# Optimization experiments

Measured on AMD Instinct MI355X. Metric: run time of the kernel, lower is better.

## Reference

```python
import jax, jax.numpy as jnp
import numpy as np

EPS = 1e-16


def setup_inputs() -> dict:
    key = jax.random.key(0)
    k1, k2 = jax.random.split(key)
    p = jax.random.normal(k1, (2, 32, 2048, 4), dtype=jnp.float32)
    q = jax.random.normal(k2, (32, 2048, 4), dtype=jnp.float32)
    return {"p": p, "q": q}


def reference(p, q):
    # im=False path: take the real part of the complex generated momenta
    p_real = p[0]                      # (B, N, 4)
    # loss_norm_choice='p3', take_sqrt=True: use 3-momenta (drop energy)
    p3 = p_real[..., 1:]               # (B, N, 3)
    q3 = q[..., 1:]                    # (B, M, 3)
    # Pairwise Euclidean distance (cdist) via the expanded quadratic form to
    # avoid materializing the (B, N, M, 3) difference tensor.
    x2 = jnp.sum(p3 * p3, axis=-1)     # (B, N)
    y2 = jnp.sum(q3 * q3, axis=-1)     # (B, M)
    xy = jnp.einsum('bnd,bmd->bnm', p3, q3)  # (B, N, M)
    dist_sq = x2[..., :, None] + y2[..., None, :] - 2.0 * xy
    dist = jnp.sqrt(jnp.maximum(dist_sq, 0.0) + EPS)  # (B, N, M)
    # Bidirectional nearest-neighbor min-reduction
    min_pq = jnp.min(dist, axis=-1)    # (B, N)
    min_qp = jnp.min(dist, axis=-2)    # (B, M)
    chamfer_loss = jnp.sum((min_pq + min_qp) * 0.5)
    return chamfer_loss
```

## Files before the change

kernel.cpp:

```cpp
#include <hip/hip_runtime.h>
#include <math.h>


#define NPTS   2048
#define NBATCH 32
#define NBI    16
#define NBJ    16
#define WS_ROW_FLOATS ((size_t)NBATCH * NBI * NBJ * 128)
#define EPSF   1e-16f
#define BIGF   3.4e38f

__device__ __forceinline__ float min3f(float a, float b, float c) {
    return fminf(fminf(a, b), c);
}

__global__ __launch_bounds__(256) void chamfer_tile_kernel(
    const float* __restrict__ P, const float* __restrict__ Q,
    float* __restrict__ ws)
{
    __shared__ float4 sq[128];
    __shared__ float  scol[4][128];
    __shared__ float  rrow[128];

    const int tid  = threadIdx.x;
    const int tx   = tid & 15;
    const int ty   = tid >> 4;
    const int lane = tid & 63;
    const int wv   = tid >> 6;
    const int bi   = blockIdx.x;
    const int bj   = blockIdx.y;
    const int b    = blockIdx.z;

    if (tid < 128) {
        float4 qv = ((const float4*)Q)[(size_t)b * NPTS + bj * 128 + tid];
        sq[tid] = make_float4(-2.f * qv.y, -2.f * qv.z, -2.f * qv.w,
                              qv.y * qv.y + qv.z * qv.z + qv.w * qv.w);
    }

    const float4* Pb = (const float4*)P + (size_t)b * NPTS + (size_t)bi * 128;
    float px[8], py[8], pz[8], x2[8], rowacc[8];
    #pragma unroll
    for (int k = 0; k < 8; ++k) {
        float4 v = Pb[ty + 16 * k];
        px[k] = v.y; py[k] = v.z; pz[k] = v.w;
        x2[k] = v.y * v.y + v.z * v.z + v.w * v.w;
        rowacc[k] = BIGF;
    }
    __syncthreads();

    float4 qr[8];
    #pragma unroll
    for (int j = 0; j < 8; ++j) qr[j] = sq[tx + 16 * j];

    float colacc[8];
    #pragma unroll
    for (int jp = 0; jp < 4; ++jp) {
        float4 q0 = qr[2 * jp];
        float4 q1 = qr[2 * jp + 1];
        float c0 = BIGF, c1 = BIGF;
        #pragma unroll
        for (int k = 0; k < 8; k += 2) {
            float t00 = fmaf(px[k],   q0.x, fmaf(py[k],   q0.y, pz[k]   * q0.z));
            float t01 = fmaf(px[k],   q1.x, fmaf(py[k],   q1.y, pz[k]   * q1.z));
            float t10 = fmaf(px[k+1], q0.x, fmaf(py[k+1], q0.y, pz[k+1] * q0.z));
            float t11 = fmaf(px[k+1], q1.x, fmaf(py[k+1], q1.y, pz[k+1] * q1.z));
            rowacc[k]   = min3f(rowacc[k],   t00 + q0.w, t01 + q1.w);
            rowacc[k+1] = min3f(rowacc[k+1], t10 + q0.w, t11 + q1.w);
            c0 = min3f(c0, t00 + x2[k], t10 + x2[k+1]);
            c1 = min3f(c1, t01 + x2[k], t11 + x2[k+1]);
        }
        colacc[2*jp]     = c0;
        colacc[2*jp + 1] = c1;
    }

    #pragma unroll
    for (int k = 0; k < 8; ++k) {
        float v = rowacc[k];
        v = fminf(v, __shfl_xor(v, 1));
        v = fminf(v, __shfl_xor(v, 2));
        v = fminf(v, __shfl_xor(v, 4));
        v = fminf(v, __shfl_xor(v, 8));
        if (tx == 0) rrow[ty + 16 * k] = x2[k] + v;
    }

    #pragma unroll
    for (int j = 0; j < 8; ++j) {
        float v = colacc[j];
        v = fminf(v, __shfl_xor(v, 16));
        v = fminf(v, __shfl_xor(v, 32));
        colacc[j] = v;
    }
    if (lane < 16) {
        #pragma unroll
        for (int j = 0; j < 8; ++j) scol[wv][j * 16 + lane] = colacc[j];
    }
    __syncthreads();

    if (tid < 128) {
        float v = fminf(fminf(scol[0][tid], scol[1][tid]),
                        fminf(scol[2][tid], scol[3][tid]));
        float* wsC = ws + WS_ROW_FLOATS;
        wsC[(((size_t)b * NBJ + bj) * NBI + bi) * 128 + tid] = v + sq[tid].w;
        ws[(((size_t)b * NBI + bi) * NBJ + bj) * 128 + tid] = rrow[tid];
    }
}

__global__ __launch_bounds__(256) void chamfer_finish_kernel(
    const float* __restrict__ ws, float* __restrict__ out)
{
    __shared__ float rbuf[4];
    const int tid = threadIdx.x;
    const int i   = blockIdx.x * 256 + tid;
    const int b   = i >> 11;
    const int e   = i & 2047;
    const int ch  = e >> 7;
    const int el  = e & 127;

    float s;
    {
        const float* rb = ws + ((size_t)(b * NBI + ch) * NBJ) * 128 + el;
        float v = BIGF;
        #pragma unroll
        for (int j = 0; j < NBJ; ++j) v = fminf(v, rb[j * 128]);
        s = sqrtf(fmaxf(v, 0.f) + EPSF);
    }
    {
        const float* cb = ws + WS_ROW_FLOATS
                        + ((size_t)(b * NBJ + ch) * NBI) * 128 + el;
        float v = BIGF;
        #pragma unroll
        for (int j = 0; j < NBI; ++j) v = fminf(v, cb[j * 128]);
        s += sqrtf(fmaxf(v, 0.f) + EPSF);
    }

    #pragma unroll
    for (int off = 32; off > 0; off >>= 1) s += __shfl_down(s, off);
    if ((tid & 63) == 0) rbuf[tid >> 6] = s;
    __syncthreads();
    if (tid == 0)
        atomicAdd(out, 0.5f * ((rbuf[0] + rbuf[1]) + (rbuf[2] + rbuf[3])));
}

extern "C" void kernel_launch(void* const* d_in, const int* in_sizes, int n_in,
                              void* d_out, int out_size, void* d_ws, size_t ws_size,
                              hipStream_t stream) {
    const float* P = (const float*)d_in[0];
    const float* Q = (const float*)d_in[1];
    float* out = (float*)d_out;
    float* ws  = (float*)d_ws;

    hipMemsetAsync(out, 0, sizeof(float), stream);
    dim3 grid(NBI, NBJ, NBATCH);
    chamfer_tile_kernel<<<grid, 256, 0, stream>>>(P, Q, ws);
    chamfer_finish_kernel<<<256, 256, 0, stream>>>(ws, out);
}
```

Measured before the change: 95.54 us.

## Loop each block over eight P tiles, keeping Q tile and column minima in registers

Each block now keeps one 128-point Q tile in registers and loops over eight P tiles (half of the points), instead of handling a single 128x128 tile. Column minima build up across the loop, so only two column partials per Q tile go to the workspace, and the finish kernel reduces two values instead of sixteen. The grid shrinks from 8192 blocks to 1024, which cuts block launch and Q reload overhead and folds x2 into the FMA chain, but lowers parallelism and serializes the P loads within each block.

```diff
diff --git a/kernel.cpp b/kernel.cpp
--- a/kernel.cpp
+++ b/kernel.cpp
@@ -6,6 +6,7 @@
 #define NBATCH 32
 #define NBI    16
 #define NBJ    16
+#define NHALF  2
 #define WS_ROW_FLOATS ((size_t)NBATCH * NBI * NBJ * 128)
 #define EPSF   1e-16f
 #define BIGF   3.4e38f
@@ -14,21 +15,20 @@
     return fminf(fminf(a, b), c);
 }
 
-__global__ __launch_bounds__(256) void chamfer_tile_kernel(
+__global__ __launch_bounds__(256, 4) void chamfer_tile_kernel(
     const float* __restrict__ P, const float* __restrict__ Q,
     float* __restrict__ ws)
 {
     __shared__ float4 sq[128];
     __shared__ float  scol[4][128];
-    __shared__ float  rrow[128];
 
     const int tid  = threadIdx.x;
     const int tx   = tid & 15;
     const int ty   = tid >> 4;
     const int lane = tid & 63;
     const int wv   = tid >> 6;
-    const int bi   = blockIdx.x;
-    const int bj   = blockIdx.y;
+    const int bj   = blockIdx.x;
+    const int half = blockIdx.y;
     const int b    = blockIdx.z;
 
     if (tid < 128) {
@@ -36,51 +36,61 @@
         sq[tid] = make_float4(-2.f * qv.y, -2.f * qv.z, -2.f * qv.w,
                               qv.y * qv.y + qv.z * qv.z + qv.w * qv.w);
     }
-
-    const float4* Pb = (const float4*)P + (size_t)b * NPTS + (size_t)bi * 128;
-    float px[8], py[8], pz[8], x2[8], rowacc[8];
-    #pragma unroll
-    for (int k = 0; k < 8; ++k) {
-        float4 v = Pb[ty + 16 * k];
-        px[k] = v.y; py[k] = v.z; pz[k] = v.w;
-        x2[k] = v.y * v.y + v.z * v.z + v.w * v.w;
-        rowacc[k] = BIGF;
-    }
     __syncthreads();
 
-    float4 qr[8];
+    float qx[8], qy[8], qz[8], qw[8], colacc[8];
     #pragma unroll
-    for (int j = 0; j < 8; ++j) qr[j] = sq[tx + 16 * j];
-
-    float colacc[8];
-    #pragma unroll
-    for (int jp = 0; jp < 4; ++jp) {
-        float4 q0 = qr[2 * jp];
-        float4 q1 = qr[2 * jp + 1];
-        float c0 = BIGF, c1 = BIGF;
-        #pragma unroll
-        for (int k = 0; k < 8; k += 2) {
-            float t00 = fmaf(px[k],   q0.x, fmaf(py[k],   q0.y, pz[k]   * q0.z));
-            float t01 = fmaf(px[k],   q1.x, fmaf(py[k],   q1.y, pz[k]   * q1.z));
-            float t10 = fmaf(px[k+1], q0.x, fmaf(py[k+1], q0.y, pz[k+1] * q0.z));
-            float t11 = fmaf(px[k+1], q1.x, fmaf(py[k+1], q1.y, pz[k+1] * q1.z));
-            rowacc[k]   = min3f(rowacc[k],   t00 + q0.w, t01 + q1.w);
-            rowacc[k+1] = min3f(rowacc[k+1], t10 + q0.w, t11 + q1.w);
-            c0 = min3f(c0, t00 + x2[k], t10 + x2[k+1]);
-            c1 = min3f(c1, t01 + x2[k], t11 + x2[k+1]);
-        }
-        colacc[2*jp]     = c0;
-        colacc[2*jp + 1] = c1;
+    for (int j = 0; j < 8; ++j) {
+        float4 t = sq[tx + 16 * j];
+        qx[j] = t.x; qy[j] = t.y; qz[j] = t.z; qw[j] = t.w;
+        colacc[j] = BIGF;
     }
 
-    #pragma unroll
-    for (int k = 0; k < 8; ++k) {
-        float v = rowacc[k];
-        v = fminf(v, __shfl_xor(v, 1));
-        v = fminf(v, __shfl_xor(v, 2));
-        v = fminf(v, __shfl_xor(v, 4));
-        v = fminf(v, __shfl_xor(v, 8));
-        if (tx == 0) rrow[ty + 16 * k] = x2[k] + v;
+    const float4* Pb = (const float4*)P + (size_t)b * NPTS
+                     + (size_t)half * (NPTS / 2);
+
+    for (int it = 0; it < 8; ++it) {
+        const int bi = half * 8 + it;
+
+        float px[8], py[8], pz[8], x2[8], rowacc[8];
+        #pragma unroll
+        for (int k = 0; k < 8; ++k) {
+            float4 v = Pb[it * 128 + ty + 16 * k];
+            px[k] = v.y; py[k] = v.z; pz[k] = v.w;
+            x2[k] = fmaf(v.y, v.y, fmaf(v.z, v.z, v.w * v.w));
+            rowacc[k] = BIGF;
+        }
+
+        #pragma unroll
+        for (int jp = 0; jp < 4; ++jp) {
+            const int j0 = 2 * jp, j1 = 2 * jp + 1;
+            #pragma unroll
+            for (int k = 0; k < 8; k += 2) {
+                float t00 = fmaf(px[k],   qx[j0], fmaf(py[k],   qy[j0], fmaf(pz[k],   qz[j0], x2[k])));
+                float t01 = fmaf(px[k],   qx[j1], fmaf(py[k],   qy[j1], fmaf(pz[k],   qz[j1], x2[k])));
+                float t10 = fmaf(px[k+1], qx[j0], fmaf(py[k+1], qy[j0], fmaf(pz[k+1], qz[j0], x2[k+1])));
+                float t11 = fmaf(px[k+1], qx[j1], fmaf(py[k+1], qy[j1], fmaf(pz[k+1], qz[j1], x2[k+1])));
+                colacc[j0] = min3f(colacc[j0], t00, t10);
+                colacc[j1] = min3f(colacc[j1], t01, t11);
+                rowacc[k]   = min3f(rowacc[k],   t00 + qw[j0], t01 + qw[j1]);
+                rowacc[k+1] = min3f(rowacc[k+1], t10 + qw[j0], t11 + qw[j1]);
+            }
+        }
+
+        #pragma unroll
+        for (int k = 0; k < 8; ++k) {
+            float v = rowacc[k];
+            v = fminf(v, __shfl_xor(v, 1));
+            v = fminf(v, __shfl_xor(v, 2));
+            v = fminf(v, __shfl_xor(v, 4));
+            v = fminf(v, __shfl_xor(v, 8));
+            rowacc[k] = v;
+        }
+        if (tx == 0) {
+            float* rb = ws + (((size_t)b * NBI + bi) * NBJ + bj) * 128;
+            #pragma unroll
+            for (int k = 0; k < 8; ++k) rb[ty + 16 * k] = rowacc[k];
+        }
     }
 
     #pragma unroll
@@ -95,13 +105,12 @@
         for (int j = 0; j < 8; ++j) scol[wv][j * 16 + lane] = colacc[j];
     }
     __syncthreads();
-
     if (tid < 128) {
         float v = fminf(fminf(scol[0][tid], scol[1][tid]),
                         fminf(scol[2][tid], scol[3][tid]));
-        float* wsC = ws + WS_ROW_FLOATS;
-        wsC[(((size_t)b * NBJ + bj) * NBI + bi) * 128 + tid] = v + sq[tid].w;
-        ws[(((size_t)b * NBI + bi) * NBJ + bj) * 128 + tid] = rrow[tid];
+        float* cb = ws + WS_ROW_FLOATS
+                  + (((size_t)b * NBJ + bj) * NHALF + half) * 128;
+        cb[tid] = v + sq[tid].w;
     }
 }
 
@@ -126,10 +135,8 @@
     }
     {
         const float* cb = ws + WS_ROW_FLOATS
-                        + ((size_t)(b * NBJ + ch) * NBI) * 128 + el;
-        float v = BIGF;
-        #pragma unroll
-        for (int j = 0; j < NBI; ++j) v = fminf(v, cb[j * 128]);
+                        + ((size_t)(b * NBJ + ch) * NHALF) * 128 + el;
+        float v = fminf(cb[0], cb[128]);
         s += sqrtf(fmaxf(v, 0.f) + EPSF);
     }
 
@@ -150,7 +157,7 @@
     float* ws  = (float*)d_ws;
 
     hipMemsetAsync(out, 0, sizeof(float), stream);
-    dim3 grid(NBI, NBJ, NBATCH);
+    dim3 grid(NBJ, NHALF, NBATCH);
     chamfer_tile_kernel<<<grid, 256, 0, stream>>>(P, Q, ws);
     chamfer_finish_kernel<<<256, 256, 0, stream>>>(ws, out);
 }
```

Measured after the change: 91.19 us. 1.05x faster.
